# Optimization experiments

Measured on AMD Instinct MI355X. Metric: run time of the kernel, lower is better.

The kernel has to match this reference:

```python
import jax, jax.numpy as jnp
import numpy as np

H, DM, DK, DV, DFF = 8, 512, 64, 64, 2048
B, S = 8, 1024
EPS = 1e-5


def layernorm_global(x):
    # torch nn.LayerNorm(x.size()[1:], elementwise_affine=False): normalize over ALL dims except batch
    mu = jnp.mean(x, axis=(1, 2), keepdims=True)
    var = jnp.var(x, axis=(1, 2), keepdims=True)
    return (x - mu) / jnp.sqrt(var + EPS)


def mha(q_in, k_in, v_in, wq, bq, wk, bk, wv, bv, wo, bo, causal):
    # wq/wk: [h, dk, dmodel], wv: [h, dv, dmodel] (torch Linear weight layout [out,in])
    q = jnp.einsum('bsd,hkd->bhsk', q_in, wq) + bq[None, :, None, :]
    k = jnp.einsum('bsd,hkd->bhsk', k_in, wk) + bk[None, :, None, :]
    v = jnp.einsum('bsd,hvd->bhsv', v_in, wv) + bv[None, :, None, :]
    scores = jnp.einsum('bhqk,bhsk->bhqs', q, k) / np.sqrt(DK).astype(np.float32)
    if causal:
        Sq = q_in.shape[1]
        mask = jnp.triu(jnp.full((Sq, Sq), -jnp.inf, dtype=scores.dtype), k=1)
        scores = scores + mask[None, None, :, :]
    w = jax.nn.softmax(scores, axis=-1)
    attn = jnp.einsum('bhqs,bhsv->bhqv', w, v)  # [b,h,q,dv]
    concat = attn.transpose(0, 2, 1, 3).reshape(q_in.shape[0], q_in.shape[1], H * DV)
    return concat @ wo.T + bo


def setup_inputs() -> dict:
    key = jax.random.key(0)
    ks = jax.random.split(key, 24)
    f = lambda k, shape: (jax.random.normal(k, shape, dtype=jnp.float32) * 0.02)
    inp = {
        'x_enc': jax.random.normal(ks[0], (B, S, DM), dtype=jnp.float32),
        'x_dec': jax.random.normal(ks[1], (B, S, DM), dtype=jnp.float32),
        # masked self-attention params
        'mq_w': f(ks[2], (H, DK, DM)), 'mq_b': f(ks[3], (H, DK)),
        'mk_w': f(ks[4], (H, DK, DM)), 'mk_b': f(ks[5], (H, DK)),
        'mv_w': f(ks[6], (H, DV, DM)), 'mv_b': f(ks[7], (H, DV)),
        'mo_w': f(ks[8], (DM, H * DV)), 'mo_b': f(ks[9], (DM,)),
        # cross-attention params
        'cq_w': f(ks[10], (H, DK, DM)), 'cq_b': f(ks[11], (H, DK)),
        'ck_w': f(ks[12], (H, DK, DM)), 'ck_b': f(ks[13], (H, DK)),
        'cv_w': f(ks[14], (H, DV, DM)), 'cv_b': f(ks[15], (H, DV)),
        'co_w': f(ks[16], (DM, H * DV)), 'co_b': f(ks[17], (DM,)),
        # feedforward params
        'f1_w': f(ks[18], (DFF, DM)), 'f1_b': f(ks[19], (DFF,)),
        'f2_w': f(ks[20], (DM, DFF)), 'f2_b': f(ks[21], (DM,)),
    }
    return inp


def reference(x_enc, x_dec,
              mq_w, mq_b, mk_w, mk_b, mv_w, mv_b, mo_w, mo_b,
              cq_w, cq_b, ck_w, ck_b, cv_w, cv_b, co_w, co_b,
              f1_w, f1_b, f2_w, f2_b):
    # masked self-attention block (dropout = identity at eval)
    x_dec_n = layernorm_global(x_dec)
    sa = mha(x_dec_n, x_dec_n, x_dec_n, mq_w, mq_b, mk_w, mk_b, mv_w, mv_b, mo_w, mo_b, causal=True)
    current = x_dec + sa
    # cross-attention block
    cur_n = layernorm_global(current)
    enc_n = layernorm_global(x_enc)
    ca = mha(cur_n, enc_n, enc_n, cq_w, cq_b, ck_w, ck_b, cv_w, cv_b, co_w, co_b, causal=False)
    result = current + ca
    # feedforward block
    res_n = layernorm_global(result)
    ff = jax.nn.relu(res_n @ f1_w.T + f1_b) @ f2_w.T + f2_b
    return result + ff
```

## Files before the change

### kernel.cpp

```cpp
#include <hip/hip_runtime.h>
#include <cmath>
#include <cstddef>
#include <cstdint>

#define BN   8
#define SN   1024
#define DMN  512
#define HN   8
#define DKN  64
#define DFFN 2048

typedef short           bf16x8   __attribute__((ext_vector_type(8)));
typedef float           f32x4    __attribute__((ext_vector_type(4)));
typedef float           f32x16   __attribute__((ext_vector_type(16)));
typedef unsigned short  ushortx4 __attribute__((ext_vector_type(4)));
typedef unsigned short  ushortx8 __attribute__((ext_vector_type(8)));
typedef unsigned int    uintx4   __attribute__((ext_vector_type(4)));
typedef unsigned short  u16;
typedef unsigned int    u32;

#define ATT_SC 0.18033688011112042f

__device__ __forceinline__ float bf2f(u16 u) {
  return __uint_as_float(((unsigned int)u) << 16);
}
__device__ __forceinline__ u16 f2bf(float f) {
  unsigned int u = __float_as_uint(f);
  u += 0x7FFFu + ((u >> 16) & 1u);
  return (u16)(u >> 16);
}
__device__ __forceinline__ u32 cvtpk_bf16(float lo, float hi) {
  u32 r;
  asm("v_cvt_pk_bf16_f32 %0, %1, %2" : "=v"(r) : "v"(lo), "v"(hi));
  return r;
}
__device__ __forceinline__ void gload_lds16(const u16* gsrc, u16* ldst) {
  __builtin_amdgcn_global_load_lds(
      (const __attribute__((address_space(1))) unsigned int*)gsrc,
      (__attribute__((address_space(3))) unsigned int*)ldst,
      16, 0, 0);
}
__device__ __forceinline__ int xcd_swz(int lid, int nwg) {
  const int cpx = nwg >> 3;
  return (lid & 7) * cpx + (lid >> 3);
}

__global__ __launch_bounds__(256) void cvt_weights(
    const float* p0, const float* p1, const float* p2, const float* p3,
    const float* p4, const float* p5, const float* p6, const float* p7,
    const float* p8, const float* p9, u16* __restrict__ dst) {
  const int gi = blockIdx.x * 256 + threadIdx.x;
  const int idx = gi * 4;
  const float* src; int off;
  if (idx < 2097152) {
    const int t = idx >> 18; off = idx & 262143;
    switch (t) {
      case 0: src = p0; break; case 1: src = p1; break;
      case 2: src = p2; break; case 3: src = p3; break;
      case 4: src = p4; break; case 5: src = p5; break;
      case 6: src = p6; break; default: src = p7; break;
    }
  } else if (idx < 3145728) { src = p8; off = idx - 2097152; }
  else                      { src = p9; off = idx - 3145728; }
  float4 v = *(const float4*)(src + off);
  ushortx4 o;
  o[0] = f2bf(v.x); o[1] = f2bf(v.y); o[2] = f2bf(v.z); o[3] = f2bf(v.w);
  *(ushortx4*)(dst + idx) = o;
}

__global__ __launch_bounds__(256) void pack_bias(const float* a, const float* b,
                                                 const float* c, const float* d,
                                                 const float* e, float* __restrict__ dst) {
  const int t = threadIdx.x;
#pragma unroll
  for (int i = t; i < 512; i += 256) {
    dst[i]        = a[i];
    dst[512 + i]  = b[i];
    dst[1024 + i] = c[i];
    dst[1536 + i] = d[i];
    dst[2048 + i] = e[i];
  }
}

template<bool INBF>
__device__ __forceinline__ void ln_sum_body(const void* Xv_, float2* part, int g, int b, int t) {
  float s = 0.f, s2 = 0.f;
  if (INBF) {
    const ushortx8* Xv = (const ushortx8*)((const u16*)Xv_ + (size_t)b * (SN * DMN) + (size_t)g * 8192);
#pragma unroll
    for (int it = 0; it < 4; ++it) {
      ushortx8 x = Xv[t + it * 256];
#pragma unroll
      for (int e = 0; e < 8; ++e) { float f = bf2f(x[e]); s += f; s2 += f * f; }
    }
  } else {
    const float4* Xv = (const float4*)((const float*)Xv_ + (size_t)b * (SN * DMN) + (size_t)g * 8192);
#pragma unroll
    for (int it = 0; it < 8; ++it) {
      float4 x = Xv[t + it * 256];
      s  += x.x + x.y + x.z + x.w;
      s2 += x.x*x.x + x.y*x.y + x.z*x.z + x.w*x.w;
    }
  }
  __shared__ float rs[256], rq[256];
  rs[t] = s; rq[t] = s2;
  __syncthreads();
  for (int off = 128; off > 0; off >>= 1) {
    if (t < off) { rs[t] += rs[t + off]; rq[t] += rq[t + off]; }
    __syncthreads();
  }
  if (t == 0) part[b * 64 + g] = make_float2(rs[0], rq[0]);
}

template<bool INBF>
__device__ __forceinline__ void ln_norm_body(const void* Xv_, const float2* part,
                                             u16* Y, int g, int b, int t) {
  __shared__ float ss[64], sq[64];
  if (t < 64) { float2 p = part[b * 64 + t]; ss[t] = p.x; sq[t] = p.y; }
  __syncthreads();
  float s = 0.f, q = 0.f;
#pragma unroll
  for (int j = 0; j < 64; ++j) { s += ss[j]; q += sq[j]; }
  const float inv_n = 1.f / (float)(SN * DMN);
  const float mu = s * inv_n;
  const float var = q * inv_n - mu * mu;
  const float rstd = rsqrtf(var + 1e-5f);
  const size_t base = (size_t)b * (SN * DMN) + (size_t)g * 8192;
  if (INBF) {
    const ushortx8* Xv = (const ushortx8*)((const u16*)Xv_ + base);
#pragma unroll
    for (int it = 0; it < 4; ++it) {
      ushortx8 x = Xv[t + it * 256];
      ushortx8 o;
#pragma unroll
      for (int e = 0; e < 8; ++e) o[e] = f2bf((bf2f(x[e]) - mu) * rstd);
      *(ushortx8*)(Y + base + (size_t)(t + it * 256) * 8) = o;
    }
  } else {
    const float4* Xv = (const float4*)((const float*)Xv_ + base);
#pragma unroll
    for (int it = 0; it < 8; ++it) {
      float4 x = Xv[t + it * 256];
      ushortx4 o;
      o[0] = f2bf((x.x - mu) * rstd); o[1] = f2bf((x.y - mu) * rstd);
      o[2] = f2bf((x.z - mu) * rstd); o[3] = f2bf((x.w - mu) * rstd);
      *(ushortx4*)(Y + base + (size_t)(t + it * 256) * 4) = o;
    }
  }
}

template<bool INBF>
__global__ __launch_bounds__(256) void ln_sum(const void* __restrict__ Xv_,
                                              float2* __restrict__ part) {
  ln_sum_body<INBF>(Xv_, part, blockIdx.x, blockIdx.y, threadIdx.x);
}
template<bool INBF>
__global__ __launch_bounds__(256) void ln_norm(const void* __restrict__ Xv_,
                                               const float2* __restrict__ part,
                                               u16* __restrict__ Y) {
  ln_norm_body<INBF>(Xv_, part, Y, blockIdx.x, blockIdx.y, threadIdx.x);
}
__global__ __launch_bounds__(256) void ln_sum2(const void* __restrict__ X0,
                                               const void* __restrict__ X1,
                                               float2* __restrict__ part) {
  if (blockIdx.z == 0) ln_sum_body<true>(X0, part, blockIdx.x, blockIdx.y, threadIdx.x);
  else                 ln_sum_body<false>(X1, part + 512, blockIdx.x, blockIdx.y, threadIdx.x);
}
__global__ __launch_bounds__(256) void ln_norm2(const void* __restrict__ X0,
                                                const void* __restrict__ X1,
                                                const float2* __restrict__ part,
                                                u16* __restrict__ Y0,
                                                u16* __restrict__ Y1) {
  if (blockIdx.z == 0) ln_norm_body<true>(X0, part, Y0, blockIdx.x, blockIdx.y, threadIdx.x);
  else                 ln_norm_body<false>(X1, part + 512, Y1, blockIdx.x, blockIdx.y, threadIdx.x);
}

template<bool RELU, bool RES, bool RESBF, int OMODE, int BM, bool QSC, bool DBUF>
__global__ __launch_bounds__(256) void gemm_mfma(const u16* __restrict__ A,
                                                 const u16* __restrict__ W,
                                                 const float* __restrict__ bias,
                                                 const void* __restrict__ resv,
                                                 void* __restrict__ Cv,
                                                 void* __restrict__ Cv2,
                                                 void* __restrict__ Cv3,
                                                 int M, int N, int K) {
  constexpr int MI = BM / 32;
  constexpr int NB = DBUF ? 2 : 1;
  __shared__ u16 As[NB][BM * 64];
  __shared__ u16 Bs[NB][128 * 64];
  const int t = threadIdx.x;
  const int lane = t & 63, w = t >> 6;
  const int wm = w >> 1, wn = w & 1;

  const int gx = gridDim.x;
  const int lid = xcd_swz(blockIdx.y * gx + blockIdx.x, gx * gridDim.y);
  const int m0 = (lid / gx) * BM, n0 = (lid % gx) * 128;

  f32x4 acc[MI][4];
#pragma unroll
  for (int i = 0; i < MI; ++i)
#pragma unroll
    for (int j = 0; j < 4; ++j)
      acc[i][j] = (f32x4){0.f, 0.f, 0.f, 0.f};

  const int srow = lane >> 3;
  const int scol = ((lane & 7) ^ (lane >> 3)) * 8;
  const int l15 = lane & 15, l4q = lane >> 4, l7 = lane & 7;

  auto STAGE = [&](int buf, int k0) {
#pragma unroll
    for (int c = 0; c < BM / 32; ++c) {
      const int r0 = c * 32 + w * 8;
      gload_lds16(A + (size_t)(m0 + r0 + srow) * K + k0 + scol, &As[buf][r0 * 64]);
    }
#pragma unroll
    for (int c = 0; c < 4; ++c) {
      const int r0 = c * 32 + w * 8;
      gload_lds16(W + (size_t)(n0 + r0 + srow) * K + k0 + scol, &Bs[buf][r0 * 64]);
    }
  };
  auto COMPUTE = [&](int buf) {
#pragma unroll
    for (int ks = 0; ks < 2; ++ks) {
      const int kofs = ((ks * 4 + l4q) ^ l7) * 8;
      bf16x8 af[MI], bfr[4];
#pragma unroll
      for (int f = 0; f < MI; ++f)
        af[f]  = *(const bf16x8*)&As[buf][(wm * (BM / 2) + f * 16 + l15) * 64 + kofs];
#pragma unroll
      for (int f = 0; f < 4; ++f)
        bfr[f] = *(const bf16x8*)&Bs[buf][(wn * 64 + f * 16 + l15) * 64 + kofs];
#pragma unroll
      for (int i = 0; i < MI; ++i)
#pragma unroll
        for (int j = 0; j < 4; ++j)
          acc[i][j] = __builtin_amdgcn_mfma_f32_16x16x32_bf16(af[i], bfr[j], acc[i][j], 0, 0, 0);
    }
  };

  if (DBUF) {
    const int nt = K >> 6;
    STAGE(0, 0);
    __syncthreads();
    for (int ti = 0; ti < nt; ++ti) {
      if (ti + 1 < nt) STAGE((ti + 1) & 1, (ti + 1) << 6);
      COMPUTE(ti & 1);
      if (ti + 1 < nt) __syncthreads();
    }
  } else {
    for (int k0 = 0; k0 < K; k0 += 64) {
      STAGE(0, k0);
      __syncthreads();
      COMPUTE(0);
      __syncthreads();
    }
  }

  const int crow0 = (lane >> 4) * 4;
  const int ccol  = lane & 15;
  float bv[4];
#pragma unroll
  for (int j = 0; j < 4; ++j) bv[j] = bias[n0 + wn * 64 + j * 16 + ccol];

  u16* seg_out = nullptr;
  int  seg_n0 = 0;
  bool seg_vt = false;
  if (OMODE == 3) {
    if (n0 < 512)       { seg_out = (u16*)Cv;  seg_n0 = 0; }
    else if (n0 < 1024) { seg_out = (u16*)Cv2; seg_n0 = 512; }
    else                { seg_out = (u16*)Cv3; seg_n0 = 1024; seg_vt = true; }
  } else if (OMODE == 4) {
    if (n0 < 512)       { seg_out = (u16*)Cv;  seg_n0 = 0; }
    else                { seg_out = (u16*)Cv3; seg_n0 = 512; seg_vt = true; }
  }
  const bool do_scale = QSC && (OMODE != 3 || n0 < 512);

#pragma unroll
  for (int i = 0; i < MI; ++i) {
#pragma unroll
    for (int r = 0; r < 4; ++r) {
      const int m = m0 + wm * (BM / 2) + i * 16 + crow0 + r;
#pragma unroll
      for (int j = 0; j < 4; ++j) {
        const int n = n0 + wn * 64 + j * 16 + ccol;
        float v = acc[i][j][r] + bv[j];
        if (RELU) v = fmaxf(v, 0.f);
        if (RES) {
          if (RESBF) v += bf2f(((const u16*)resv)[(size_t)m * N + n]);
          else       v += ((const float*)resv)[(size_t)m * N + n];
        }
        if (do_scale) v *= ATT_SC;
        if (OMODE == 0) {
          ((float*)Cv)[(size_t)m * N + n] = v;
        } else if (OMODE == 1) {
          ((u16*)Cv)[(size_t)m * N + n] = f2bf(v);
        } else {
          const int nn = n - seg_n0;
          if (!seg_vt) seg_out[(size_t)m * 512 + nn] = f2bf(v);
          else
            seg_out[(((size_t)(m >> 10) * HN + (nn >> 6)) * 64 + (nn & 63)) * SN + (m & 1023)] = f2bf(v);
        }
      }
    }
  }
}

#define QBLK 128
#define KVB  64

template<int CAUSAL, int NSPLIT>
__global__ __launch_bounds__(256) void attn_mfma(const u16* __restrict__ Q,
                                                 const u16* __restrict__ K,
                                                 const u16* __restrict__ VT,
                                                 u16* __restrict__ Out,
                                                 float* __restrict__ Lbuf) {
  const int lid = xcd_swz(blockIdx.y * 8 + blockIdx.x, 512);
  const int qb = lid & 7;
  const int bh = lid >> 3;
  const int sp = (NSPLIT > 1) ? blockIdx.z : 0;
  const int b = bh >> 3, h = bh & 7;
  const int t = threadIdx.x;
  const int lane = t & 63, w = t >> 6;
  const int l31 = lane & 31, hi = lane >> 5;

  __shared__ __align__(16) u16 Ks[2][64 * 64];
  __shared__ __align__(16) u16 Vts[2][8 * 512];

  const int qw0 = qb * QBLK + w * 32;
  const int qglob = qw0 + l31;

  bf16x8 bq[4];
#pragma unroll
  for (int dk = 0; dk < 4; ++dk)
    bq[dk] = *(const bf16x8*)(Q + (size_t)(b * SN + qglob) * 512
                                + h * 64 + dk * 16 + hi * 8);

  f32x16 acc0 = {}, acc1 = {};
  float l_run = 0.f;

  const int ntile = CAUSAL ? (2 * qb + 2) : (SN / KVB);
  const int n4 = (ntile + NSPLIT - 1) / NSPLIT;
  const int kt0 = sp * n4;
  const int ktend = (kt0 + n4 < ntile) ? (kt0 + n4) : ntile;
  const int ntk = ktend - kt0;

  const int srow = t >> 2;
  const int ss0  = 2 * (t & 3);
  const u16* kg0 = K + (size_t)(b * SN + srow) * 512 + h * 64 + ((ss0 ^ (srow & 7)) * 8)
                     + (size_t)kt0 * KVB * 512;
  const u16* kg1 = K + (size_t)(b * SN + srow) * 512 + h * 64 + (((ss0 + 1) ^ (srow & 7)) * 8)
                     + (size_t)kt0 * KVB * 512;
  const int vd = t & 63, vp = t >> 6;
  const u16* vg = VT + ((size_t)bh * 64 + vd) * SN + vp * 16 + kt0 * KVB;

  ushortx8 kr0, kr1, vr0, vr1;
  auto LOADREGS = [&]() {
    kr0 = *(const ushortx8*)kg0;
    kr1 = *(const ushortx8*)kg1;
    vr0 = *(const ushortx8*)vg;
    vr1 = *(const ushortx8*)(vg + 8);
    kg0 += (size_t)KVB * 512; kg1 += (size_t)KVB * 512; vg += KVB;
  };
  auto WRITELDS = [&](int buf) {
    *(ushortx8*)&Ks[buf][t * 16]     = kr0;
    *(ushortx8*)&Ks[buf][t * 16 + 8] = kr1;
    ushortx8 sl, sh;
#pragma unroll
    for (int e = 0; e < 4; ++e) {
      sl[e] = vr0[e];     sl[e + 4] = vr1[e];
      sh[e] = vr0[e + 4]; sh[e + 4] = vr1[e + 4];
    }
    *(ushortx8*)&Vts[buf][(2 * vp) * 512 + vd * 8]     = sl;
    *(ushortx8*)&Vts[buf][(2 * vp + 1) * 512 + vd * 8] = sh;
  };

  LOADREGS();
  WRITELDS(0);
  if (ntk > 1) LOADREGS();
  __syncthreads();

  for (int ti = 0; ti < ntk; ++ti) {
    const int kt = kt0 + ti;
    const int k0 = kt * KVB;
    const int cur = ti & 1;
    if (ti + 1 < ntk) {
      WRITELDS(cur ^ 1);
      if (ti + 2 < ntk) LOADREGS();
    }

    if (!(CAUSAL && k0 > qw0 + 31)) {
      f32x16 s0 = {}, s1 = {};
      __builtin_amdgcn_s_setprio(1);
#pragma unroll
      for (int dk = 0; dk < 4; ++dk) {
        const int boff = dk * 32 + hi * 16;
        const int sw = boff ^ ((l31 & 7) << 4);
        bf16x8 a0 = *(const bf16x8*)&Ks[cur][l31 * 64 + (sw >> 1)];
        bf16x8 a1 = *(const bf16x8*)&Ks[cur][(32 + l31) * 64 + (sw >> 1)];
        s0 = __builtin_amdgcn_mfma_f32_32x32x16_bf16(a0, bq[dk], s0, 0, 0, 0);
        s1 = __builtin_amdgcn_mfma_f32_32x32x16_bf16(a1, bq[dk], s1, 0, 0, 0);
      }
      __builtin_amdgcn_s_setprio(0);

      if (CAUSAL && (k0 + KVB - 1 > qw0)) {
#pragma unroll
        for (int i = 0; i < 16; ++i) {
          const int krow = (i & 3) + 8 * (i >> 2) + 4 * hi;
          if (k0 + krow > qglob)      s0[i] = -INFINITY;
          if (k0 + 32 + krow > qglob) s1[i] = -INFINITY;
        }
      }
      float ps = 0.f;
#pragma unroll
      for (int i = 0; i < 16; ++i) {
        s0[i] = exp2f(s0[i]); ps += s0[i];
        s1[i] = exp2f(s1[i]); ps += s1[i];
      }
      l_run += ps;

      __builtin_amdgcn_s_setprio(1);
#pragma unroll
      for (int m = 0; m < 4; ++m) {
        uintx4 pw;
        if (m == 0) {
          pw[0] = cvtpk_bf16(s0[0], s0[1]);  pw[1] = cvtpk_bf16(s0[2], s0[3]);
          pw[2] = cvtpk_bf16(s0[4], s0[5]);  pw[3] = cvtpk_bf16(s0[6], s0[7]);
        } else if (m == 1) {
          pw[0] = cvtpk_bf16(s0[8], s0[9]);  pw[1] = cvtpk_bf16(s0[10], s0[11]);
          pw[2] = cvtpk_bf16(s0[12], s0[13]); pw[3] = cvtpk_bf16(s0[14], s0[15]);
        } else if (m == 2) {
          pw[0] = cvtpk_bf16(s1[0], s1[1]);  pw[1] = cvtpk_bf16(s1[2], s1[3]);
          pw[2] = cvtpk_bf16(s1[4], s1[5]);  pw[3] = cvtpk_bf16(s1[6], s1[7]);
        } else {
          pw[0] = cvtpk_bf16(s1[8], s1[9]);  pw[1] = cvtpk_bf16(s1[10], s1[11]);
          pw[2] = cvtpk_bf16(s1[12], s1[13]); pw[3] = cvtpk_bf16(s1[14], s1[15]);
        }
        const bf16x8 pb = *(const bf16x8*)&pw;
        const bf16x8 av0 = *(const bf16x8*)&Vts[cur][(m * 2 + hi) * 512 + l31 * 8];
        const bf16x8 av1 = *(const bf16x8*)&Vts[cur][(m * 2 + hi) * 512 + (32 + l31) * 8];
        acc0 = __builtin_amdgcn_mfma_f32_32x32x16_bf16(av0, pb, acc0, 0, 0, 0);
        acc1 = __builtin_amdgcn_mfma_f32_32x32x16_bf16(av1, pb, acc1, 0, 0, 0);
      }
      __builtin_amdgcn_s_setprio(0);
    }
    if (ti + 1 < ntk) __syncthreads();
  }

  l_run += __shfl_xor(l_run, 32);
  if (NSPLIT == 1) {
    const float inv = 1.f / l_run;
    u16* op = Out + (size_t)(b * SN + qglob) * 512 + h * 64;
#pragma unroll
    for (int g = 0; g < 4; ++g) {
      ushortx4 o0, o1;
#pragma unroll
      for (int r = 0; r < 4; ++r) {
        o0[r] = f2bf(acc0[4*g + r] * inv);
        o1[r] = f2bf(acc1[4*g + r] * inv);
      }
      *(ushortx4*)(op + 4*hi + 8*g)      = o0;
      *(ushortx4*)(op + 32 + 4*hi + 8*g) = o1;
    }
  } else {
    u16* op = Out + (((size_t)(sp * 64 + bh)) * 1024 + qglob) * 64;
#pragma unroll
    for (int g = 0; g < 4; ++g) {
      ushortx4 o0, o1;
#pragma unroll
      for (int r = 0; r < 4; ++r) {
        o0[r] = f2bf(acc0[4*g + r]);
        o1[r] = f2bf(acc1[4*g + r]);
      }
      *(ushortx4*)(op + 4*hi + 8*g)      = o0;
      *(ushortx4*)(op + 32 + 4*hi + 8*g) = o1;
    }
    if (hi == 0)
      Lbuf[((size_t)(sp * 64 + bh)) * 1024 + qglob] = l_run;
  }
}

__global__ __launch_bounds__(256) void attn_merge2(const u16* __restrict__ Pacc,
                                                   const float* __restrict__ Lbuf,
                                                   u16* __restrict__ O) {
  const int tid = blockIdx.x * 256 + threadIdx.x;
  const int qh = tid >> 3;
  const int d0 = (tid & 7) * 8;
  const int bh = qh >> 10, q = qh & 1023;
  const int b = bh >> 3, h = bh & 7;

  const float l = Lbuf[(size_t)bh * 1024 + q] + Lbuf[(size_t)(64 + bh) * 1024 + q];
  const float inv = 1.f / l;
  ushortx8 a0 = *(const ushortx8*)(Pacc + ((size_t)bh * 1024 + q) * 64 + d0);
  ushortx8 a1 = *(const ushortx8*)(Pacc + ((size_t)(64 + bh) * 1024 + q) * 64 + d0);
  ushortx8 ov;
#pragma unroll
  for (int e = 0; e < 8; ++e)
    ov[e] = f2bf((bf2f(a0[e]) + bf2f(a1[e])) * inv);
  *(ushortx8*)(O + ((size_t)(b * 1024 + q) * 512) + h * 64 + d0) = ov;
}

extern "C" void kernel_launch(void* const* d_in, const int* in_sizes, int n_in,
                              void* d_out, int out_size, void* d_ws, size_t ws_size,
                              hipStream_t stream) {
  const float* x_enc = (const float*)d_in[0];
  const float* x_dec = (const float*)d_in[1];
  const float* mq_w = (const float*)d_in[2];  const float* mq_b = (const float*)d_in[3];
  const float* mk_w = (const float*)d_in[4];  const float* mk_b = (const float*)d_in[5];
  const float* mv_w = (const float*)d_in[6];  const float* mv_b = (const float*)d_in[7];
  const float* mo_w = (const float*)d_in[8];  const float* mo_b = (const float*)d_in[9];
  const float* cq_w = (const float*)d_in[10]; const float* cq_b = (const float*)d_in[11];
  const float* ck_w = (const float*)d_in[12]; const float* ck_b = (const float*)d_in[13];
  const float* cv_w = (const float*)d_in[14]; const float* cv_b = (const float*)d_in[15];
  const float* co_w = (const float*)d_in[16]; const float* co_b = (const float*)d_in[17];
  const float* f1_w = (const float*)d_in[18]; const float* f1_b = (const float*)d_in[19];
  const float* f2_w = (const float*)d_in[20]; const float* f2_b = (const float*)d_in[21];
  float* out = (float*)d_out;

  char* wsb = (char*)d_ws;
  u16* o5    = (u16*)(wsb + 0);
  u16* o6    = (u16*)(wsb + (16u << 20));
  u16* Qb    = (u16*)(wsb + (32u << 20));
  u16* Kb    = (u16*)(wsb + (40u << 20));
  u16* VTb   = (u16*)(wsb + (48u << 20));
  u16* B0    = (u16*)(wsb + (56u << 20));
  u16* B1    = (u16*)(wsb + (64u << 20));
  u16* FF1   = (u16*)(wsb + (72u << 20));
  u16* WB    = (u16*)(wsb + (104u << 20));
  float2* part = (float2*)(wsb + (112u << 20));
  float* BC  = (float*)(wsb + (113u << 20));

  u16* Pacc   = FF1;
  float* Lbuf = (float*)B1;

  u16* wb_mq = WB + 0 * 262144;
  u16* wb_mo = WB + 3 * 262144;
  u16* wb_cq = WB + 4 * 262144;
  u16* wb_ck = WB + 5 * 262144;
  u16* wb_co = WB + 7 * 262144;
  u16* wb_f1 = WB + 8 * 262144; u16* wb_f2 = WB + 8 * 262144 + 1048576;

  const int M = BN * SN;
  dim3 ln_grid(64, BN);
  dim3 ln_grid2(64, BN, 2);
  dim3 g512s(512 / 128, M / 64);
  dim3 g1024(1024 / 128, M / 128);
  dim3 g1536(1536 / 128, M / 128);
  dim3 g2048(2048 / 128, M / 128);
  dim3 attn_grid_c(SN / QBLK, BN * HN, 2);
  dim3 attn_grid_x(SN / QBLK, BN * HN, 1);

  cvt_weights<<<4096, 256, 0, stream>>>(mq_w, mk_w, mv_w, mo_w, cq_w, ck_w, cv_w, co_w,
                                        f1_w, f2_w, WB);
  pack_bias<<<1, 256, 0, stream>>>(mq_b, mk_b, mv_b, ck_b, cv_b, BC);

  ln_sum<false><<<ln_grid, 256, 0, stream>>>(x_dec, part);
  ln_norm<false><<<ln_grid, 256, 0, stream>>>(x_dec, part, B0);
  gemm_mfma<false, false, false, 3, 128, true, false><<<g1536, 256, 0, stream>>>(
      B0, wb_mq, BC, nullptr, Qb, Kb, VTb, M, 1536, 512);
  attn_mfma<1, 2><<<attn_grid_c, 256, 0, stream>>>(Qb, Kb, VTb, Pacc, Lbuf);
  attn_merge2<<<2048, 256, 0, stream>>>(Pacc, Lbuf, B0);
  gemm_mfma<false, true, false, 1, 64, false, true><<<g512s, 256, 0, stream>>>(
      B0, wb_mo, mo_b, x_dec, o5, nullptr, nullptr, M, 512, 512);

  ln_sum2<<<ln_grid2, 256, 0, stream>>>(o5, x_enc, part);
  ln_norm2<<<ln_grid2, 256, 0, stream>>>(o5, x_enc, part, B0, B1);
  gemm_mfma<false, false, false, 1, 64, true, true><<<g512s, 256, 0, stream>>>(
      B0, wb_cq, cq_b, nullptr, Qb, nullptr, nullptr, M, 512, 512);
  gemm_mfma<false, false, false, 4, 128, false, false><<<g1024, 256, 0, stream>>>(
      B1, wb_ck, BC + 1536, nullptr, Kb, nullptr, VTb, M, 1024, 512);
  attn_mfma<0, 1><<<attn_grid_x, 256, 0, stream>>>(Qb, Kb, VTb, B0, nullptr);
  gemm_mfma<false, true, true, 1, 64, false, true><<<g512s, 256, 0, stream>>>(
      B0, wb_co, co_b, o5, o6, nullptr, nullptr, M, 512, 512);

  ln_sum<true><<<ln_grid, 256, 0, stream>>>(o6, part);
  ln_norm<true><<<ln_grid, 256, 0, stream>>>(o6, part, B0);
  gemm_mfma<true, false, false, 1, 128, false, false><<<g2048, 256, 0, stream>>>(
      B0, wb_f1, f1_b, nullptr, FF1, nullptr, nullptr, M, 2048, 512);
  gemm_mfma<false, true, true, 0, 64, false, true><<<g512s, 256, 0, stream>>>(
      FF1, wb_f2, f2_b, o6, out, nullptr, nullptr, M, 512, 2048);
}
```

Baseline: 253.9 us.

## Pre-permute V^T into attention LDS layout and shrink GEMM M-tiles

The QKV/KV GEMM epilogue now writes V^T in a blocked layout that already matches the attention kernel's shared-memory arrangement. The attention kernel can then copy V tiles straight into LDS with no register shuffle. Separately, the GEMM M-tile sizes are halved across the projection, output and FF2 GEMMs, which launches more blocks. The scattered epilogue stores may coalesce less well, and smaller tiles reduce data reuse.

Result: faster. 245.5 us, median of 2 (-3.3%).

```diff
diff --git a/kernel.cpp b/kernel.cpp
--- a/kernel.cpp
+++ b/kernel.cpp
@@ -296,9 +296,15 @@
           ((u16*)Cv)[(size_t)m * N + n] = f2bf(v);
         } else {
           const int nn = n - seg_n0;
-          if (!seg_vt) seg_out[(size_t)m * 512 + nn] = f2bf(v);
-          else
-            seg_out[(((size_t)(m >> 10) * HN + (nn >> 6)) * 64 + (nn & 63)) * SN + (m & 1023)] = f2bf(v);
+          if (!seg_vt) {
+            seg_out[(size_t)m * 512 + nn] = f2bf(v);
+          } else {
+            const int s_ = m & 1023, k_ = s_ & 63;
+            const int slab = 4 * (k_ >> 5) + 2 * ((k_ >> 4) & 1) + ((k_ >> 2) & 1);
+            const int jj   = 4 * ((k_ >> 3) & 1) + (k_ & 3);
+            seg_out[(((((size_t)(m >> 10) * HN + (nn >> 6)) * 16 + (s_ >> 6)) * 8 + slab) * 64
+                     + (nn & 63)) * 8 + jj] = f2bf(v);
+          }
         }
       }
     }
@@ -311,7 +317,7 @@
 template<int CAUSAL, int NSPLIT>
 __global__ __launch_bounds__(256) void attn_mfma(const u16* __restrict__ Q,
                                                  const u16* __restrict__ K,
-                                                 const u16* __restrict__ VT,
+                                                 const u16* __restrict__ VTp,
                                                  u16* __restrict__ Out,
                                                  float* __restrict__ Lbuf) {
   const int lid = xcd_swz(blockIdx.y * 8 + blockIdx.x, 512);
@@ -351,27 +357,21 @@
   const u16* kg1 = K + (size_t)(b * SN + srow) * 512 + h * 64 + (((ss0 + 1) ^ (srow & 7)) * 8)
                      + (size_t)kt0 * KVB * 512;
   const int vd = t & 63, vp = t >> 6;
-  const u16* vg = VT + ((size_t)bh * 64 + vd) * SN + vp * 16 + kt0 * KVB;
+  const u16* vg = VTp + (((size_t)bh * 16 + kt0) * 8 + 2 * vp) * 512 + vd * 8;
 
   ushortx8 kr0, kr1, vr0, vr1;
   auto LOADREGS = [&]() {
     kr0 = *(const ushortx8*)kg0;
     kr1 = *(const ushortx8*)kg1;
     vr0 = *(const ushortx8*)vg;
-    vr1 = *(const ushortx8*)(vg + 8);
-    kg0 += (size_t)KVB * 512; kg1 += (size_t)KVB * 512; vg += KVB;
+    vr1 = *(const ushortx8*)(vg + 512);
+    kg0 += (size_t)KVB * 512; kg1 += (size_t)KVB * 512; vg += 4096;
   };
   auto WRITELDS = [&](int buf) {
     *(ushortx8*)&Ks[buf][t * 16]     = kr0;
     *(ushortx8*)&Ks[buf][t * 16 + 8] = kr1;
-    ushortx8 sl, sh;
-#pragma unroll
-    for (int e = 0; e < 4; ++e) {
-      sl[e] = vr0[e];     sl[e + 4] = vr1[e];
-      sh[e] = vr0[e + 4]; sh[e + 4] = vr1[e + 4];
-    }
-    *(ushortx8*)&Vts[buf][(2 * vp) * 512 + vd * 8]     = sl;
-    *(ushortx8*)&Vts[buf][(2 * vp + 1) * 512 + vd * 8] = sh;
+    *(ushortx8*)&Vts[buf][(2 * vp) * 512 + vd * 8]     = vr0;
+    *(ushortx8*)&Vts[buf][(2 * vp + 1) * 512 + vd * 8] = vr1;
   };
 
   LOADREGS();
@@ -542,9 +542,9 @@
   const int M = BN * SN;
   dim3 ln_grid(64, BN);
   dim3 ln_grid2(64, BN, 2);
-  dim3 g512s(512 / 128, M / 64);
-  dim3 g1024(1024 / 128, M / 128);
-  dim3 g1536(1536 / 128, M / 128);
+  dim3 g512t(512 / 128, M / 32);
+  dim3 gqkv(1536 / 128, M / 64);
+  dim3 gkv(1024 / 128, M / 64);
   dim3 g2048(2048 / 128, M / 128);
   dim3 attn_grid_c(SN / QBLK, BN * HN, 2);
   dim3 attn_grid_x(SN / QBLK, BN * HN, 1);
@@ -555,27 +555,27 @@
 
   ln_sum<false><<<ln_grid, 256, 0, stream>>>(x_dec, part);
   ln_norm<false><<<ln_grid, 256, 0, stream>>>(x_dec, part, B0);
-  gemm_mfma<false, false, false, 3, 128, true, false><<<g1536, 256, 0, stream>>>(
+  gemm_mfma<false, false, false, 3, 64, true, false><<<gqkv, 256, 0, stream>>>(
       B0, wb_mq, BC, nullptr, Qb, Kb, VTb, M, 1536, 512);
   attn_mfma<1, 2><<<attn_grid_c, 256, 0, stream>>>(Qb, Kb, VTb, Pacc, Lbuf);
   attn_merge2<<<2048, 256, 0, stream>>>(Pacc, Lbuf, B0);
-  gemm_mfma<false, true, false, 1, 64, false, true><<<g512s, 256, 0, stream>>>(
+  gemm_mfma<false, true, false, 1, 32, false, true><<<g512t, 256, 0, stream>>>(
       B0, wb_mo, mo_b, x_dec, o5, nullptr, nullptr, M, 512, 512);
 
   ln_sum2<<<ln_grid2, 256, 0, stream>>>(o5, x_enc, part);
   ln_norm2<<<ln_grid2, 256, 0, stream>>>(o5, x_enc, part, B0, B1);
-  gemm_mfma<false, false, false, 1, 64, true, true><<<g512s, 256, 0, stream>>>(
+  gemm_mfma<false, false, false, 1, 32, true, true><<<g512t, 256, 0, stream>>>(
       B0, wb_cq, cq_b, nullptr, Qb, nullptr, nullptr, M, 512, 512);
-  gemm_mfma<false, false, false, 4, 128, false, false><<<g1024, 256, 0, stream>>>(
+  gemm_mfma<false, false, false, 4, 64, false, false><<<gkv, 256, 0, stream>>>(
       B1, wb_ck, BC + 1536, nullptr, Kb, nullptr, VTb, M, 1024, 512);
   attn_mfma<0, 1><<<attn_grid_x, 256, 0, stream>>>(Qb, Kb, VTb, B0, nullptr);
-  gemm_mfma<false, true, true, 1, 64, false, true><<<g512s, 256, 0, stream>>>(
+  gemm_mfma<false, true, true, 1, 32, false, true><<<g512t, 256, 0, stream>>>(
       B0, wb_co, co_b, o5, o6, nullptr, nullptr, M, 512, 512);
 
   ln_sum<true><<<ln_grid, 256, 0, stream>>>(o6, part);
   ln_norm<true><<<ln_grid, 256, 0, stream>>>(o6, part, B0);
   gemm_mfma<true, false, false, 1, 128, false, false><<<g2048, 256, 0, stream>>>(
       B0, wb_f1, f1_b, nullptr, FF1, nullptr, nullptr, M, 2048, 512);
-  gemm_mfma<false, true, true, 0, 64, false, true><<<g512s, 256, 0, stream>>>(
+  gemm_mfma<false, true, true, 0, 32, false, true><<<g512t, 256, 0, stream>>>(
       FF1, wb_f2, f2_b, o6, out, nullptr, nullptr, M, 512, 2048);
 }
```
